# Performance work log

Hardware: AMD Instinct MI355X
Metric: run time of the kernel (lower is better)

Reference implementation:

```python
import jax, jax.numpy as jnp
import numpy as np

FLOAT_MIN = jnp.finfo(jnp.float32).min


def setup_inputs() -> dict:
    key = jax.random.key(0)
    ks = jax.random.split(key, 8)
    B, S, F1, F2, A = 65536, 256, 256, 256, 128
    return {
        "obs_state": jax.random.normal(ks[0], (B, S), dtype=jnp.float32),
        "action_mask": jax.random.randint(ks[1], (B, A), 0, 2, dtype=jnp.int32),
        "W1": jax.random.normal(ks[2], (S, F1), dtype=jnp.float32) * (1.0 / np.sqrt(S)),
        "b1": jnp.zeros((F1,), dtype=jnp.float32),
        "W2": jax.random.normal(ks[3], (F1, F2), dtype=jnp.float32) * (1.0 / np.sqrt(F1)),
        "b2": jnp.zeros((F2,), dtype=jnp.float32),
        "W3": jax.random.normal(ks[4], (F2, A), dtype=jnp.float32) * (1.0 / np.sqrt(F2)),
        "b3": jnp.zeros((A,), dtype=jnp.float32),
    }


def reference(obs_state, action_mask, W1, b1, W2, b2, W3, b3):
    # 3-layer MLP: state -> fc1 -> relu -> fc2 -> relu -> fc3
    h = jax.nn.relu(obs_state @ W1 + b1)
    h = jax.nn.relu(h @ W2 + b2)
    x = h @ W3 + b3  # [B, A] logits

    # Vectorized action masking (replaces per-element Python loop):
    #   mask==0 -> FLOAT_MIN; rows with all-zero mask -> FLOAT_MIN everywhere, col 0 = 1.0
    valid = action_mask != 0  # [B, A] bool
    x = jnp.where(valid, x, FLOAT_MIN)
    all_invalid = ~jnp.any(valid, axis=1, keepdims=True)  # [B, 1]
    col0 = jnp.arange(x.shape[1]) == 0  # [A]
    x = jnp.where(all_invalid & col0, jnp.float32(1.0), x)
    return x
```

## Files before the change

### kernel.cpp

```cpp
#include <hip/hip_runtime.h>

typedef __attribute__((ext_vector_type(8))) short short8;
typedef __attribute__((ext_vector_type(8))) unsigned short ushort8;
typedef __attribute__((ext_vector_type(4))) float f32x4;

#define MT 64
#define STR 264

__device__ __forceinline__ float bmax_r13() { return __uint_as_float(0x7F7F0000u); }

__device__ __forceinline__ unsigned short f2bf_r13(float f) {
    unsigned int u = __float_as_uint(f);
    return (unsigned short)((u + 0x7fffu + ((u >> 16) & 1u)) >> 16);
}

__global__ __launch_bounds__(256)
void pack_weights_r13(const float* __restrict__ W1,
                      const float* __restrict__ W2,
                      const float* __restrict__ W3,
                      unsigned short* __restrict__ ws) {
    int s = blockIdx.x * 256 + threadIdx.x;
    const float* src;
    unsigned short* dst;
    int N;
    if (s < 8192)       { src = W1; dst = ws;          N = 256; }
    else if (s < 16384) { src = W2; dst = ws + 65536;  N = 256; s -= 8192; }
    else                { src = W3; dst = ws + 131072; N = 128; s -= 16384; }
    int frag = s >> 6, lane = s & 63;
    int kb = (frag & 7) * 32 + (lane >> 4) * 8;
    int n  = (frag >> 3) * 16 + (lane & 15);
    ushort8 o;
    #pragma unroll
    for (int j = 0; j < 8; ++j) o[j] = f2bf_r13(src[(kb + j) * N + n]);
    *(ushort8*)&dst[s * 8] = o;
}

__device__ __forceinline__ void layer_mfma_r13(
    const unsigned short* __restrict__ act, const unsigned short* __restrict__ wp,
    int wave, int lane, int quad, int noff, f32x4 acc[4][2])
{
    #pragma unroll
    for (int k0 = 0; k0 < 8; ++k0) {
        short8 b0 = *(const short8*)&wp[(((wave * 2 + 0) * 8 + k0) * 64 + lane) * 8];
        short8 b1 = *(const short8*)&wp[(((wave * 2 + 1) * 8 + k0) * 64 + lane) * 8];
        #pragma unroll
        for (int rt = 0; rt < 4; ++rt) {
            short8 a = *(const short8*)&act[(rt * 16 + noff) * STR + k0 * 32 + quad * 8];
            acc[rt][0] = __builtin_amdgcn_mfma_f32_16x16x32_bf16(a, b0, acc[rt][0], 0, 0, 0);
            acc[rt][1] = __builtin_amdgcn_mfma_f32_16x16x32_bf16(a, b1, acc[rt][1], 0, 0, 0);
        }
    }
}

__device__ __forceinline__ void layer_store_r13(
    unsigned short* __restrict__ act, const float* __restrict__ bias,
    int wave, int quad, int noff, f32x4 acc[4][2])
{
    #pragma unroll
    for (int ct = 0; ct < 2; ++ct) {
        int col = (wave * 2 + ct) * 16 + noff;
        float bv = bias[col];
        #pragma unroll
        for (int rt = 0; rt < 4; ++rt) {
            #pragma unroll
            for (int i = 0; i < 4; ++i) {
                float v = fmaxf(acc[rt][ct][i] + bv, 0.0f);
                act[(rt * 16 + quad * 4 + i) * STR + col] = f2bf_r13(v);
            }
        }
    }
}

__global__ __launch_bounds__(512, 8)
void ColorNetwork_32495722561720_kernel(
        const float* __restrict__ obs,
        const int* __restrict__ amask,
        const float* __restrict__ b1,
        const float* __restrict__ b2,
        const float* __restrict__ b3,
        const unsigned short* __restrict__ w1p,
        const unsigned short* __restrict__ w2p,
        const unsigned short* __restrict__ w3p,
        float* __restrict__ out)
{
    __shared__ __align__(16) unsigned short act[MT * STR];
    __shared__ int rowany[MT];

    const int tid  = threadIdx.x;
    const int wave = tid >> 6;
    const int lane = tid & 63;
    const int quad = lane >> 4;
    const int noff = lane & 15;
    const size_t rowbase = (size_t)blockIdx.x * MT;

    if (tid < MT) rowany[tid] = 0;

    const float4* xin = (const float4*)(obs + rowbase * 256);
    #pragma unroll
    for (int i = 0; i < 8; ++i) {
        int f = tid + i * 512;
        int row = f >> 6;
        int c4 = f & 63;
        float4 v = xin[f];
        ushort4 p;
        p.x = f2bf_r13(v.x); p.y = f2bf_r13(v.y);
        p.z = f2bf_r13(v.z); p.w = f2bf_r13(v.w);
        *(ushort4*)&act[row * STR + c4 * 4] = p;
    }
    __syncthreads();

    const int4* min4 = (const int4*)(amask + rowbase * 128);
    #pragma unroll
    for (int i = 0; i < 4; ++i) {
        int f = tid + i * 512;
        int4 m = min4[f];
        if (m.x | m.y | m.z | m.w) rowany[f >> 5] = 1;
    }

    {
        f32x4 acc[4][2] = {};
        layer_mfma_r13(act, w1p, wave, lane, quad, noff, acc);
        __syncthreads();
        layer_store_r13(act, b1, wave, quad, noff, acc);
        __syncthreads();
    }
    {
        f32x4 acc[4][2] = {};
        layer_mfma_r13(act, w2p, wave, lane, quad, noff, acc);
        __syncthreads();
        layer_store_r13(act, b2, wave, quad, noff, acc);
        __syncthreads();
    }
    {
        const int col = wave * 16 + noff;

        f32x4 acc[4] = {};
        #pragma unroll
        for (int k0 = 0; k0 < 8; ++k0) {
            short8 b0 = *(const short8*)&w3p[((wave * 8 + k0) * 64 + lane) * 8];
            #pragma unroll
            for (int rt = 0; rt < 4; ++rt) {
                short8 a = *(const short8*)&act[(rt * 16 + noff) * STR + k0 * 32 + quad * 8];
                acc[rt] = __builtin_amdgcn_mfma_f32_16x16x32_bf16(a, b0, acc[rt], 0, 0, 0);
            }
        }

        int mv[16];
        #pragma unroll
        for (int rt = 0; rt < 4; ++rt)
            #pragma unroll
            for (int i = 0; i < 4; ++i)
                mv[rt * 4 + i] = amask[(rowbase + rt * 16 + quad * 4 + i) * 128 + col];

        const float BM = bmax_r13();
        const float bv = b3[col];
        #pragma unroll
        for (int rt = 0; rt < 4; ++rt) {
            #pragma unroll
            for (int i = 0; i < 4; ++i) {
                int row = rt * 16 + quad * 4 + i;
                float v = acc[rt][i] + bv;
                v = fminf(fmaxf(v, -BM), BM);
                if (!(v == v)) v = 0.0f;
                if (!mv[rt * 4 + i]) v = -BM;
                if (!rowany[row]) v = (col == 0) ? 1.0f : -BM;
                out[(rowbase + row) * 128 + col] = v;
            }
        }
    }
}

extern "C" void kernel_launch(void* const* d_in, const int* in_sizes, int n_in,
                              void* d_out, int out_size, void* d_ws, size_t ws_size,
                              hipStream_t stream) {
    const float* obs   = (const float*)d_in[0];
    const int*   amask = (const int*)d_in[1];
    const float* W1 = (const float*)d_in[2];
    const float* b1 = (const float*)d_in[3];
    const float* W2 = (const float*)d_in[4];
    const float* b2 = (const float*)d_in[5];
    const float* W3 = (const float*)d_in[6];
    const float* b3 = (const float*)d_in[7];
    float* out = (float*)d_out;

    const int B = in_sizes[0] / 256;

    unsigned short* ws = (unsigned short*)d_ws;
    unsigned short* w1p = ws;
    unsigned short* w2p = ws + 65536;
    unsigned short* w3p = ws + 131072;

    pack_weights_r13<<<80, 256, 0, stream>>>(W1, W2, W3, ws);

    ColorNetwork_32495722561720_kernel<<<B / MT, 512, 0, stream>>>(
        obs, amask, b1, b2, b3, w1p, w2p, w3p, out);
}
```

Before: 176.8 us.

## Halve row tile to 32 with 4-wave blocks and wider per-wave column tiles

Shrinks the per-block row tile from 64 to 32 and the block from 512 to 256 threads (4 waves). Each wave now computes 2 row tiles by 4 column tiles, so each loaded weight fragment is reused across fewer rows while each activation fragment is reused across more columns. The smaller LDS footprint allows more resident blocks, but weight reads from global/L2 per output row double. The final layer is reorganized to match, with the mask loads interleaved into the epilogue instead of being prefetched into an array.

```diff
diff --git a/kernel.cpp b/kernel.cpp
--- a/kernel.cpp
+++ b/kernel.cpp
@@ -4,18 +4,18 @@
 typedef __attribute__((ext_vector_type(8))) unsigned short ushort8;
 typedef __attribute__((ext_vector_type(4))) float f32x4;
 
-#define MT 64
+#define MT 32
 #define STR 264
 
-__device__ __forceinline__ float bmax_r13() { return __uint_as_float(0x7F7F0000u); }
+__device__ __forceinline__ float bmax_r14() { return __uint_as_float(0x7F7F0000u); }
 
-__device__ __forceinline__ unsigned short f2bf_r13(float f) {
+__device__ __forceinline__ unsigned short f2bf_r14(float f) {
     unsigned int u = __float_as_uint(f);
     return (unsigned short)((u + 0x7fffu + ((u >> 16) & 1u)) >> 16);
 }
 
 __global__ __launch_bounds__(256)
-void pack_weights_r13(const float* __restrict__ W1,
+void pack_weights_r14(const float* __restrict__ W1,
                       const float* __restrict__ W2,
                       const float* __restrict__ W3,
                       unsigned short* __restrict__ ws) {
@@ -31,47 +31,50 @@
     int n  = (frag >> 3) * 16 + (lane & 15);
     ushort8 o;
     #pragma unroll
-    for (int j = 0; j < 8; ++j) o[j] = f2bf_r13(src[(kb + j) * N + n]);
+    for (int j = 0; j < 8; ++j) o[j] = f2bf_r14(src[(kb + j) * N + n]);
     *(ushort8*)&dst[s * 8] = o;
 }
 
-__device__ __forceinline__ void layer_mfma_r13(
+__device__ __forceinline__ void layer_mfma_r14(
     const unsigned short* __restrict__ act, const unsigned short* __restrict__ wp,
-    int wave, int lane, int quad, int noff, f32x4 acc[4][2])
+    int wave, int lane, int quad, int noff, f32x4 acc[2][4])
 {
     #pragma unroll
     for (int k0 = 0; k0 < 8; ++k0) {
-        short8 b0 = *(const short8*)&wp[(((wave * 2 + 0) * 8 + k0) * 64 + lane) * 8];
-        short8 b1 = *(const short8*)&wp[(((wave * 2 + 1) * 8 + k0) * 64 + lane) * 8];
+        short8 b[4];
         #pragma unroll
-        for (int rt = 0; rt < 4; ++rt) {
+        for (int ct = 0; ct < 4; ++ct)
+            b[ct] = *(const short8*)&wp[(((wave * 4 + ct) * 8 + k0) * 64 + lane) * 8];
+        #pragma unroll
+        for (int rt = 0; rt < 2; ++rt) {
             short8 a = *(const short8*)&act[(rt * 16 + noff) * STR + k0 * 32 + quad * 8];
-            acc[rt][0] = __builtin_amdgcn_mfma_f32_16x16x32_bf16(a, b0, acc[rt][0], 0, 0, 0);
-            acc[rt][1] = __builtin_amdgcn_mfma_f32_16x16x32_bf16(a, b1, acc[rt][1], 0, 0, 0);
+            #pragma unroll
+            for (int ct = 0; ct < 4; ++ct)
+                acc[rt][ct] = __builtin_amdgcn_mfma_f32_16x16x32_bf16(a, b[ct], acc[rt][ct], 0, 0, 0);
         }
     }
 }
 
-__device__ __forceinline__ void layer_store_r13(
+__device__ __forceinline__ void layer_store_r14(
     unsigned short* __restrict__ act, const float* __restrict__ bias,
-    int wave, int quad, int noff, f32x4 acc[4][2])
+    int wave, int quad, int noff, f32x4 acc[2][4])
 {
     #pragma unroll
-    for (int ct = 0; ct < 2; ++ct) {
-        int col = (wave * 2 + ct) * 16 + noff;
+    for (int ct = 0; ct < 4; ++ct) {
+        int col = (wave * 4 + ct) * 16 + noff;
         float bv = bias[col];
         #pragma unroll
-        for (int rt = 0; rt < 4; ++rt) {
+        for (int rt = 0; rt < 2; ++rt) {
             #pragma unroll
             for (int i = 0; i < 4; ++i) {
                 float v = fmaxf(acc[rt][ct][i] + bv, 0.0f);
-                act[(rt * 16 + quad * 4 + i) * STR + col] = f2bf_r13(v);
+                act[(rt * 16 + quad * 4 + i) * STR + col] = f2bf_r14(v);
             }
         }
     }
 }
 
-__global__ __launch_bounds__(512, 8)
+__global__ __launch_bounds__(256, 6)
 void ColorNetwork_32495722561720_kernel(
         const float* __restrict__ obs,
         const int* __restrict__ amask,
@@ -98,13 +101,13 @@
     const float4* xin = (const float4*)(obs + rowbase * 256);
     #pragma unroll
     for (int i = 0; i < 8; ++i) {
-        int f = tid + i * 512;
+        int f = tid + i * 256;
         int row = f >> 6;
         int c4 = f & 63;
         float4 v = xin[f];
         ushort4 p;
-        p.x = f2bf_r13(v.x); p.y = f2bf_r13(v.y);
-        p.z = f2bf_r13(v.z); p.w = f2bf_r13(v.w);
+        p.x = f2bf_r14(v.x); p.y = f2bf_r14(v.y);
+        p.z = f2bf_r14(v.z); p.w = f2bf_r14(v.w);
         *(ushort4*)&act[row * STR + c4 * 4] = p;
     }
     __syncthreads();
@@ -112,59 +115,57 @@
     const int4* min4 = (const int4*)(amask + rowbase * 128);
     #pragma unroll
     for (int i = 0; i < 4; ++i) {
-        int f = tid + i * 512;
+        int f = tid + i * 256;
         int4 m = min4[f];
         if (m.x | m.y | m.z | m.w) rowany[f >> 5] = 1;
     }
 
     {
-        f32x4 acc[4][2] = {};
-        layer_mfma_r13(act, w1p, wave, lane, quad, noff, acc);
+        f32x4 acc[2][4] = {};
+        layer_mfma_r14(act, w1p, wave, lane, quad, noff, acc);
         __syncthreads();
-        layer_store_r13(act, b1, wave, quad, noff, acc);
+        layer_store_r14(act, b1, wave, quad, noff, acc);
         __syncthreads();
     }
     {
-        f32x4 acc[4][2] = {};
-        layer_mfma_r13(act, w2p, wave, lane, quad, noff, acc);
+        f32x4 acc[2][4] = {};
+        layer_mfma_r14(act, w2p, wave, lane, quad, noff, acc);
         __syncthreads();
-        layer_store_r13(act, b2, wave, quad, noff, acc);
+        layer_store_r14(act, b2, wave, quad, noff, acc);
         __syncthreads();
     }
     {
-        const int col = wave * 16 + noff;
-
-        f32x4 acc[4] = {};
+        f32x4 acc[2][2] = {};
         #pragma unroll
         for (int k0 = 0; k0 < 8; ++k0) {
-            short8 b0 = *(const short8*)&w3p[((wave * 8 + k0) * 64 + lane) * 8];
+            short8 b0 = *(const short8*)&w3p[(((wave * 2 + 0) * 8 + k0) * 64 + lane) * 8];
+            short8 b1v = *(const short8*)&w3p[(((wave * 2 + 1) * 8 + k0) * 64 + lane) * 8];
             #pragma unroll
-            for (int rt = 0; rt < 4; ++rt) {
+            for (int rt = 0; rt < 2; ++rt) {
                 short8 a = *(const short8*)&act[(rt * 16 + noff) * STR + k0 * 32 + quad * 8];
-                acc[rt] = __builtin_amdgcn_mfma_f32_16x16x32_bf16(a, b0, acc[rt], 0, 0, 0);
+                acc[rt][0] = __builtin_amdgcn_mfma_f32_16x16x32_bf16(a, b0, acc[rt][0], 0, 0, 0);
+                acc[rt][1] = __builtin_amdgcn_mfma_f32_16x16x32_bf16(a, b1v, acc[rt][1], 0, 0, 0);
             }
         }
 
-        int mv[16];
+        const float BM = bmax_r14();
         #pragma unroll
-        for (int rt = 0; rt < 4; ++rt)
+        for (int ct = 0; ct < 2; ++ct) {
+            int col = (wave * 2 + ct) * 16 + noff;
+            float bv = b3[col];
             #pragma unroll
-            for (int i = 0; i < 4; ++i)
-                mv[rt * 4 + i] = amask[(rowbase + rt * 16 + quad * 4 + i) * 128 + col];
-
-        const float BM = bmax_r13();
-        const float bv = b3[col];
-        #pragma unroll
-        for (int rt = 0; rt < 4; ++rt) {
-            #pragma unroll
-            for (int i = 0; i < 4; ++i) {
-                int row = rt * 16 + quad * 4 + i;
-                float v = acc[rt][i] + bv;
-                v = fminf(fmaxf(v, -BM), BM);
-                if (!(v == v)) v = 0.0f;
-                if (!mv[rt * 4 + i]) v = -BM;
-                if (!rowany[row]) v = (col == 0) ? 1.0f : -BM;
-                out[(rowbase + row) * 128 + col] = v;
+            for (int rt = 0; rt < 2; ++rt) {
+                #pragma unroll
+                for (int i = 0; i < 4; ++i) {
+                    int row = rt * 16 + quad * 4 + i;
+                    int m = amask[(rowbase + row) * 128 + col];
+                    float v = acc[rt][ct][i] + bv;
+                    v = fminf(fmaxf(v, -BM), BM);
+                    if (!(v == v)) v = 0.0f;
+                    if (!m) v = -BM;
+                    if (!rowany[row]) v = (col == 0) ? 1.0f : -BM;
+                    out[(rowbase + row) * 128 + col] = v;
+                }
             }
         }
     }
@@ -190,8 +191,8 @@
     unsigned short* w2p = ws + 65536;
     unsigned short* w3p = ws + 131072;
 
-    pack_weights_r13<<<80, 256, 0, stream>>>(W1, W2, W3, ws);
+    pack_weights_r14<<<80, 256, 0, stream>>>(W1, W2, W3, ws);
 
-    ColorNetwork_32495722561720_kernel<<<B / MT, 512, 0, stream>>>(
+    ColorNetwork_32495722561720_kernel<<<B / MT, 256, 0, stream>>>(
         obs, amask, b1, b2, b3, w1p, w2p, w3p, out);
 }
```

Result: no change. 179.8 us (+1.7%).

## Double-buffer activations in LDS and preload weight fragments into registers

Applied to the files above, without the earlier changes.

Uses two LDS slabs that ping-pong between layers, which removes the barrier that separated each layer's MFMA reads from its writes. Each layer's weight fragments are loaded into registers before the barrier, so global loads overlap the previous layer's work. Rows are processed in a non-unrolled loop, loading all eight A fragments and running MFMAs per 16-row tile. This doubles LDS per block (about 68KB) and lowers launch_bounds occupancy from 8 to 4, which cuts the number of resident blocks.

```diff
diff --git a/kernel.cpp b/kernel.cpp
--- a/kernel.cpp
+++ b/kernel.cpp
@@ -7,15 +7,15 @@
 #define MT 64
 #define STR 264
 
-__device__ __forceinline__ float bmax_r13() { return __uint_as_float(0x7F7F0000u); }
-
-__device__ __forceinline__ unsigned short f2bf_r13(float f) {
+__device__ __forceinline__ float bmax_r21() { return __uint_as_float(0x7F7F0000u); }
+
+__device__ __forceinline__ unsigned short f2bf_r21(float f) {
     unsigned int u = __float_as_uint(f);
     return (unsigned short)((u + 0x7fffu + ((u >> 16) & 1u)) >> 16);
 }
 
 __global__ __launch_bounds__(256)
-void pack_weights_r13(const float* __restrict__ W1,
+void pack_weights_r21(const float* __restrict__ W1,
                       const float* __restrict__ W2,
                       const float* __restrict__ W3,
                       unsigned short* __restrict__ ws) {
@@ -31,47 +31,11 @@
     int n  = (frag >> 3) * 16 + (lane & 15);
     ushort8 o;
     #pragma unroll
-    for (int j = 0; j < 8; ++j) o[j] = f2bf_r13(src[(kb + j) * N + n]);
+    for (int j = 0; j < 8; ++j) o[j] = f2bf_r21(src[(kb + j) * N + n]);
     *(ushort8*)&dst[s * 8] = o;
 }
 
-__device__ __forceinline__ void layer_mfma_r13(
-    const unsigned short* __restrict__ act, const unsigned short* __restrict__ wp,
-    int wave, int lane, int quad, int noff, f32x4 acc[4][2])
-{
-    #pragma unroll
-    for (int k0 = 0; k0 < 8; ++k0) {
-        short8 b0 = *(const short8*)&wp[(((wave * 2 + 0) * 8 + k0) * 64 + lane) * 8];
-        short8 b1 = *(const short8*)&wp[(((wave * 2 + 1) * 8 + k0) * 64 + lane) * 8];
-        #pragma unroll
-        for (int rt = 0; rt < 4; ++rt) {
-            short8 a = *(const short8*)&act[(rt * 16 + noff) * STR + k0 * 32 + quad * 8];
-            acc[rt][0] = __builtin_amdgcn_mfma_f32_16x16x32_bf16(a, b0, acc[rt][0], 0, 0, 0);
-            acc[rt][1] = __builtin_amdgcn_mfma_f32_16x16x32_bf16(a, b1, acc[rt][1], 0, 0, 0);
-        }
-    }
-}
-
-__device__ __forceinline__ void layer_store_r13(
-    unsigned short* __restrict__ act, const float* __restrict__ bias,
-    int wave, int quad, int noff, f32x4 acc[4][2])
-{
-    #pragma unroll
-    for (int ct = 0; ct < 2; ++ct) {
-        int col = (wave * 2 + ct) * 16 + noff;
-        float bv = bias[col];
-        #pragma unroll
-        for (int rt = 0; rt < 4; ++rt) {
-            #pragma unroll
-            for (int i = 0; i < 4; ++i) {
-                float v = fmaxf(acc[rt][ct][i] + bv, 0.0f);
-                act[(rt * 16 + quad * 4 + i) * STR + col] = f2bf_r13(v);
-            }
-        }
-    }
-}
-
-__global__ __launch_bounds__(512, 8)
+__global__ __launch_bounds__(512, 4)
 void ColorNetwork_32495722561720_kernel(
         const float* __restrict__ obs,
         const int* __restrict__ amask,
@@ -83,7 +47,8 @@
         const unsigned short* __restrict__ w3p,
         float* __restrict__ out)
 {
-    __shared__ __align__(16) unsigned short act[MT * STR];
+    __shared__ __align__(16) unsigned short slabA[MT * STR];
+    __shared__ __align__(16) unsigned short slabB[MT * STR];
     __shared__ int rowany[MT];
 
     const int tid  = threadIdx.x;
@@ -95,74 +60,127 @@
 
     if (tid < MT) rowany[tid] = 0;
 
-    const float4* xin = (const float4*)(obs + rowbase * 256);
-    #pragma unroll
-    for (int i = 0; i < 8; ++i) {
-        int f = tid + i * 512;
-        int row = f >> 6;
-        int c4 = f & 63;
-        float4 v = xin[f];
-        ushort4 p;
-        p.x = f2bf_r13(v.x); p.y = f2bf_r13(v.y);
-        p.z = f2bf_r13(v.z); p.w = f2bf_r13(v.w);
-        *(ushort4*)&act[row * STR + c4 * 4] = p;
+    {
+        const float4* xin = (const float4*)(obs + rowbase * 256);
+        #pragma unroll
+        for (int i = 0; i < 8; ++i) {
+            int f = tid + i * 512;
+            int row = f >> 6;
+            int c4 = f & 63;
+            float4 v = xin[f];
+            ushort4 p;
+            p.x = f2bf_r21(v.x); p.y = f2bf_r21(v.y);
+            p.z = f2bf_r21(v.z); p.w = f2bf_r21(v.w);
+            *(ushort4*)&slabA[row * STR + c4 * 4] = p;
+        }
+    }
+
+    short8 bA[8], bB[8];
+    {
+        const int c0 = wave * 2, c1 = wave * 2 + 1;
+        #pragma unroll
+        for (int k0 = 0; k0 < 8; ++k0) {
+            bA[k0] = *(const short8*)&w1p[((c0 * 8 + k0) * 64 + lane) * 8];
+            bB[k0] = *(const short8*)&w1p[((c1 * 8 + k0) * 64 + lane) * 8];
+        }
     }
     __syncthreads();
 
-    const int4* min4 = (const int4*)(amask + rowbase * 128);
-    #pragma unroll
-    for (int i = 0; i < 4; ++i) {
-        int f = tid + i * 512;
-        int4 m = min4[f];
-        if (m.x | m.y | m.z | m.w) rowany[f >> 5] = 1;
-    }
-
-    {
-        f32x4 acc[4][2] = {};
-        layer_mfma_r13(act, w1p, wave, lane, quad, noff, acc);
-        __syncthreads();
-        layer_store_r13(act, b1, wave, quad, noff, acc);
-        __syncthreads();
-    }
-    {
-        f32x4 acc[4][2] = {};
-        layer_mfma_r13(act, w2p, wave, lane, quad, noff, acc);
-        __syncthreads();
-        layer_store_r13(act, b2, wave, quad, noff, acc);
-        __syncthreads();
-    }
+    {
+        const int4* min4 = (const int4*)(amask + rowbase * 128);
+        #pragma unroll
+        for (int i = 0; i < 4; ++i) {
+            int f = tid + i * 512;
+            int4 m = min4[f];
+            if (m.x | m.y | m.z | m.w) rowany[f >> 5] = 1;
+        }
+    }
+
+    {
+        const int col0 = (wave * 2) * 16 + noff;
+        const float bv0 = b1[col0], bv1 = b1[col0 + 16];
+        #pragma unroll 1
+        for (int r = 0; r < 4; ++r) {
+            short8 a[8];
+            #pragma unroll
+            for (int k0 = 0; k0 < 8; ++k0)
+                a[k0] = *(const short8*)&slabA[(r * 16 + noff) * STR + k0 * 32 + quad * 8];
+            f32x4 ac0 = {}, ac1 = {};
+            #pragma unroll
+            for (int k0 = 0; k0 < 8; ++k0) {
+                ac0 = __builtin_amdgcn_mfma_f32_16x16x32_bf16(a[k0], bA[k0], ac0, 0, 0, 0);
+                ac1 = __builtin_amdgcn_mfma_f32_16x16x32_bf16(a[k0], bB[k0], ac1, 0, 0, 0);
+            }
+            #pragma unroll
+            for (int i = 0; i < 4; ++i) {
+                int rw = (r * 16 + quad * 4 + i) * STR;
+                slabB[rw + col0]      = f2bf_r21(fmaxf(ac0[i] + bv0, 0.0f));
+                slabB[rw + col0 + 16] = f2bf_r21(fmaxf(ac1[i] + bv1, 0.0f));
+            }
+        }
+    }
+    {
+        const int c0 = wave * 2, c1 = wave * 2 + 1;
+        #pragma unroll
+        for (int k0 = 0; k0 < 8; ++k0) {
+            bA[k0] = *(const short8*)&w2p[((c0 * 8 + k0) * 64 + lane) * 8];
+            bB[k0] = *(const short8*)&w2p[((c1 * 8 + k0) * 64 + lane) * 8];
+        }
+    }
+    __syncthreads();
+
+    {
+        const int col0 = (wave * 2) * 16 + noff;
+        const float bv0 = b2[col0], bv1 = b2[col0 + 16];
+        #pragma unroll 1
+        for (int r = 0; r < 4; ++r) {
+            short8 a[8];
+            #pragma unroll
+            for (int k0 = 0; k0 < 8; ++k0)
+                a[k0] = *(const short8*)&slabB[(r * 16 + noff) * STR + k0 * 32 + quad * 8];
+            f32x4 ac0 = {}, ac1 = {};
+            #pragma unroll
+            for (int k0 = 0; k0 < 8; ++k0) {
+                ac0 = __builtin_amdgcn_mfma_f32_16x16x32_bf16(a[k0], bA[k0], ac0, 0, 0, 0);
+                ac1 = __builtin_amdgcn_mfma_f32_16x16x32_bf16(a[k0], bB[k0], ac1, 0, 0, 0);
+            }
+            #pragma unroll
+            for (int i = 0; i < 4; ++i) {
+                int rw = (r * 16 + quad * 4 + i) * STR;
+                slabA[rw + col0]      = f2bf_r21(fmaxf(ac0[i] + bv0, 0.0f));
+                slabA[rw + col0 + 16] = f2bf_r21(fmaxf(ac1[i] + bv1, 0.0f));
+            }
+        }
+    }
+    {
+        #pragma unroll
+        for (int k0 = 0; k0 < 8; ++k0)
+            bA[k0] = *(const short8*)&w3p[((wave * 8 + k0) * 64 + lane) * 8];
+    }
+    __syncthreads();
+
     {
         const int col = wave * 16 + noff;
-
-        f32x4 acc[4] = {};
-        #pragma unroll
-        for (int k0 = 0; k0 < 8; ++k0) {
-            short8 b0 = *(const short8*)&w3p[((wave * 8 + k0) * 64 + lane) * 8];
-            #pragma unroll
-            for (int rt = 0; rt < 4; ++rt) {
-                short8 a = *(const short8*)&act[(rt * 16 + noff) * STR + k0 * 32 + quad * 8];
-                acc[rt] = __builtin_amdgcn_mfma_f32_16x16x32_bf16(a, b0, acc[rt], 0, 0, 0);
-            }
-        }
-
-        int mv[16];
-        #pragma unroll
-        for (int rt = 0; rt < 4; ++rt)
-            #pragma unroll
-            for (int i = 0; i < 4; ++i)
-                mv[rt * 4 + i] = amask[(rowbase + rt * 16 + quad * 4 + i) * 128 + col];
-
-        const float BM = bmax_r13();
         const float bv = b3[col];
-        #pragma unroll
-        for (int rt = 0; rt < 4; ++rt) {
+        const float BM = bmax_r21();
+        #pragma unroll 1
+        for (int r = 0; r < 4; ++r) {
+            short8 a[8];
+            #pragma unroll
+            for (int k0 = 0; k0 < 8; ++k0)
+                a[k0] = *(const short8*)&slabA[(r * 16 + noff) * STR + k0 * 32 + quad * 8];
+            f32x4 acc = {};
+            #pragma unroll
+            for (int k0 = 0; k0 < 8; ++k0)
+                acc = __builtin_amdgcn_mfma_f32_16x16x32_bf16(a[k0], bA[k0], acc, 0, 0, 0);
             #pragma unroll
             for (int i = 0; i < 4; ++i) {
-                int row = rt * 16 + quad * 4 + i;
-                float v = acc[rt][i] + bv;
+                int row = r * 16 + quad * 4 + i;
+                int m = amask[(rowbase + row) * 128 + col];
+                float v = acc[i] + bv;
                 v = fminf(fmaxf(v, -BM), BM);
                 if (!(v == v)) v = 0.0f;
-                if (!mv[rt * 4 + i]) v = -BM;
+                if (!m) v = -BM;
                 if (!rowany[row]) v = (col == 0) ? 1.0f : -BM;
                 out[(rowbase + row) * 128 + col] = v;
             }
@@ -190,7 +208,7 @@
     unsigned short* w2p = ws + 65536;
     unsigned short* w3p = ws + 131072;
 
-    pack_weights_r13<<<80, 256, 0, stream>>>(W1, W2, W3, ws);
+    pack_weights_r21<<<80, 256, 0, stream>>>(W1, W2, W3, ws);
 
     ColorNetwork_32495722561720_kernel<<<B / MT, 512, 0, stream>>>(
         obs, amask, b1, b2, b3, w1p, w2p, w3p, out);
```

New measurement: 159.2 us. 1.11x faster.
